# Kernel tuning notes

Measured on AMD Instinct MI355X. Metric: run time of the kernel, lower is better.

The kernel has to match this reference:

```python
import jax, jax.numpy as jnp
import numpy as np
from jax import lax

H = 64  # hidden size


def _lstm_layer(x, w_ih, w_hh, b_ih, b_hh):
    """Single LSTM layer, batch_first x: [B, T, D] -> [B, T, H].
    PyTorch gate order: i, f, g, o."""
    B = x.shape[0]
    # Precompute input projections for all timesteps: [T, B, 4H]
    xg = jnp.einsum('btd,gd->tbg', x, w_ih) + (b_ih + b_hh)

    def step(carry, xg_t):
        h, c = carry
        gates = xg_t + h @ w_hh.T  # [B, 4H]
        i, f, g, o = jnp.split(gates, 4, axis=-1)
        i = jax.nn.sigmoid(i)
        f = jax.nn.sigmoid(f)
        g = jnp.tanh(g)
        o = jax.nn.sigmoid(o)
        c = f * c + i * g
        h = o * jnp.tanh(c)
        return (h, c), h

    h0 = jnp.zeros((B, H), dtype=x.dtype)
    c0 = jnp.zeros((B, H), dtype=x.dtype)
    (_, _), hs = lax.scan(step, (h0, c0), xg)  # hs: [T, B, H]
    return jnp.swapaxes(hs, 0, 1)  # [B, T, H]


def setup_inputs() -> dict:
    key = jax.random.key(0)
    ks = jax.random.split(key, 11)
    s = 1.0 / np.sqrt(H)  # PyTorch LSTM init scale
    x = jax.random.normal(ks[0], (8192, 168, 7), dtype=jnp.float32)
    return {
        'x': x,
        'w_ih0': jax.random.normal(ks[1], (4 * H, 7), jnp.float32) * s,
        'w_hh0': jax.random.normal(ks[2], (4 * H, H), jnp.float32) * s,
        'b_ih0': jax.random.normal(ks[3], (4 * H,), jnp.float32) * s,
        'b_hh0': jax.random.normal(ks[4], (4 * H,), jnp.float32) * s,
        'w_ih1': jax.random.normal(ks[5], (4 * H, H), jnp.float32) * s,
        'w_hh1': jax.random.normal(ks[6], (4 * H, H), jnp.float32) * s,
        'b_ih1': jax.random.normal(ks[7], (4 * H,), jnp.float32) * s,
        'b_hh1': jax.random.normal(ks[8], (4 * H,), jnp.float32) * s,
        'fc_w': jax.random.normal(ks[9], (4, H), jnp.float32) * s,
        'fc_b': jax.random.normal(ks[10], (4,), jnp.float32) * s,
    }


def reference(x, w_ih0, w_hh0, b_ih0, b_hh0, w_ih1, w_hh1, b_ih1, b_hh1, fc_w, fc_b):
    h1 = _lstm_layer(x, w_ih0, w_hh0, b_ih0, b_hh0)   # [B, T, H]
    h2 = _lstm_layer(h1, w_ih1, w_hh1, b_ih1, b_hh1)  # [B, T, H]
    last = h2[:, -1, :]                               # dropout is identity in eval
    return last @ fc_w.T + fc_b                       # [B, 4]
```

## Files before the change

### kernel.cpp

```cpp
#include <hip/hip_runtime.h>

#define TT 168
#define HH 64
#define DD 7
#define NS 16
#define BB 8192
#define CH 8
#define NTH 512

typedef float f32x2 __attribute__((ext_vector_type(2)));
typedef float f32x4 __attribute__((ext_vector_type(4)));
typedef _Float16 f16x8 __attribute__((ext_vector_type(8)));

#define MFMA16F(A, B, C) __builtin_amdgcn_mfma_f32_16x16x32_f16((A), (B), (C), 0, 0, 0)

__device__ __forceinline__ f16x8 pack8(f32x4 a, f32x4 b) {
    f16x8 r;
#pragma unroll
    for (int e = 0; e < 4; ++e) { r[e] = (_Float16)a[e]; r[4 + e] = (_Float16)b[e]; }
    return r;
}

__device__ __forceinline__ f32x2 exp2x2(f32x2 a) {
    return (f32x2){__builtin_amdgcn_exp2f(fminf(a.x, 40.0f)),
                   __builtin_amdgcn_exp2f(fminf(a.y, 40.0f))};
}
__device__ __forceinline__ f32x2 rcpx2(f32x2 a) {
    return (f32x2){__builtin_amdgcn_rcpf(a.x), __builtin_amdgcn_rcpf(a.y)};
}

__device__ __forceinline__ void cell_pair(f32x2 si, f32x2 sf, f32x2 sg, f32x2 so,
                                          f32x2& cs, unsigned& dpk) {
    const f32x2 one = {1.0f, 1.0f};
    const f32x2 ui  = exp2x2(si);
    const f32x2 uf  = exp2x2(sf);
    const f32x2 ug  = exp2x2(sg);
    const f32x2 opf = one + uf;
    const f32x2 pig = (one + ui) * (one + ug);
    const f32x2 R1  = rcpx2(pig * opf);
    const f32x2 fv  = pig * R1;
    const f32x2 igs = (ug * 2.88539008f - (f32x2){2.88539008f, 2.88539008f}) * (opf * R1);
    cs = fv * cs + igs;
    const f32x2 uo = exp2x2(so);
    const f32x2 uc = exp2x2(cs);
    const f32x2 R2 = rcpx2((one + uo) * (one + uc));
    const f32x2 hv = (one - uc) * R2;
    asm("v_cvt_pkrtz_f16_f32 %0, %1, %2" : "=v"(dpk) : "v"(hv.x), "v"(hv.y));
}

__device__ __forceinline__ void cell_update(const f32x4& gi, const f32x4& gf,
                                            const f32x4& gg, const f32x4& go,
                                            f32x4& cs, _Float16* dst) {
    f32x2 csA = {cs[0], cs[1]}, csB = {cs[2], cs[3]};
    unsigned d0, d1;
    cell_pair((f32x2){gi[0], gi[1]}, (f32x2){gf[0], gf[1]},
              (f32x2){gg[0], gg[1]}, (f32x2){go[0], go[1]}, csA, d0);
    cell_pair((f32x2){gi[2], gi[3]}, (f32x2){gf[2], gf[3]},
              (f32x2){gg[2], gg[3]}, (f32x2){go[2], go[3]}, csB, d1);
    cs[0] = csA.x; cs[1] = csA.y; cs[2] = csB.x; cs[3] = csB.y;
    *(uint2*)dst = make_uint2(d0, d1);
}

__global__ __launch_bounds__(NTH, 4)
void weather_lstm_mfma(const float* __restrict__ x,
                       const float* __restrict__ w_ih0, const float* __restrict__ w_hh0,
                       const float* __restrict__ b_ih0, const float* __restrict__ b_hh0,
                       const float* __restrict__ w_ih1, const float* __restrict__ w_hh1,
                       const float* __restrict__ b_ih1, const float* __restrict__ b_hh1,
                       const float* __restrict__ fc_w, const float* __restrict__ fc_b,
                       float* __restrict__ out)
{
    __shared__ f16x8 xs[2][CH][4][NS];
    __shared__ __align__(16) _Float16 h1[2][NS][72];
    __shared__ __align__(16) _Float16 h2[2][NS][72];

    const int tid  = threadIdx.x;
    const int wv   = tid >> 6;
    const int q    = wv & 3;
    const int lane = tid & 63;
    const int col  = lane & 15;
    const int kg   = lane >> 4;
    const int s0   = blockIdx.x * NS;
    const int ub   = 16 * q + 4 * kg;

    for (int i = tid; i < 2 * NS * 72; i += NTH) {
        ((short*)h1)[i] = 0; ((short*)h2)[i] = 0;
    }
    {
        const f16x8 z8i = {0, 0, 0, 0, 0, 0, 0, 0};
        f16x8* xf = &xs[0][0][0][0];
        for (int i = tid; i < 2 * CH * 4 * NS; i += NTH) xf[i] = z8i;
    }
    __syncthreads();
    if (tid < CH * NS) {
        const int tloc = tid >> 4, ss = tid & 15;
        const float* px = x + ((size_t)(s0 + ss) * TT + tloc) * DD;
        f32x4 a, b;
        a[0] = px[0]; a[1] = px[1]; a[2] = px[2]; a[3] = px[3];
        b[0] = px[4]; b[1] = px[5]; b[2] = px[6]; b[3] = 1.0f;
        xs[0][tloc][0][ss] = pack8(a, b);
    }
    __syncthreads();

    const f32x4 zz = {0, 0, 0, 0};

    if (wv < 4) {
        f16x8 W0[4][2], WX[4];
#pragma unroll
        for (int t4 = 0; t4 < 4; ++t4) {
            const float sc = (t4 == 2) ? -2.88539008f : -1.44269504f;
            const int row = 64 * t4 + 16 * q + col;
#pragma unroll
            for (int kf = 0; kf < 2; ++kf) {
                const float* p = w_hh0 + (size_t)row * HH + 32 * kf + 8 * kg;
                W0[t4][kf] = pack8(*(const f32x4*)p * sc, *(const f32x4*)(p + 4) * sc);
            }
            f32x4 a = {0, 0, 0, 0}, b = {0, 0, 0, 0};
            if (kg == 0) {
                const float* p = w_ih0 + (size_t)row * DD;
                a[0] = p[0]; a[1] = p[1]; a[2] = p[2]; a[3] = p[3];
                b[0] = p[4]; b[1] = p[5]; b[2] = p[6];
                b[3] = b_ih0[row] + b_hh0[row];
            }
            WX[t4] = pack8(a * sc, b * sc);
        }
        f32x4 c1 = {0, 0, 0, 0};

        const f16x8* xk = &xs[0][0][kg][col];
        const _Float16* r0a = &h1[0][col][8 * kg];
        const _Float16* r0b = &h1[0][col][32 + 8 * kg];
        const _Float16* r1a = &h1[1][col][8 * kg];
        const _Float16* r1b = &h1[1][col][32 + 8 * kg];
        _Float16* wp0 = &h1[0][col][ub];
        _Float16* wp1 = &h1[1][col][ub];

        auto l0_step = [&](int xofs, const _Float16* ra, const _Float16* rb,
                           _Float16* wr) {
            f32x4 a0, a1, a2, a3;
            const f16x8 ax = xk[xofs];
            a0 = MFMA16F(WX[0], ax, zz);
            a1 = MFMA16F(WX[1], ax, zz);
            a2 = MFMA16F(WX[2], ax, zz);
            a3 = MFMA16F(WX[3], ax, zz);
            f16x8 dh = *(const f16x8*)ra;
            a0 = MFMA16F(W0[0][0], dh, a0);
            a1 = MFMA16F(W0[1][0], dh, a1);
            a2 = MFMA16F(W0[2][0], dh, a2);
            a3 = MFMA16F(W0[3][0], dh, a3);
            dh = *(const f16x8*)rb;
            a0 = MFMA16F(W0[0][1], dh, a0);
            a1 = MFMA16F(W0[1][1], dh, a1);
            a2 = MFMA16F(W0[2][1], dh, a2);
            a3 = MFMA16F(W0[3][1], dh, a3);
            cell_update(a0, a1, a2, a3, c1, wr);
        };
        auto refill = [&](int kref) {
            if (tid < CH * NS) {
                const int tloc = tid >> 4, ss = tid & 15;
                const int tg = kref + CH + tloc;
                const float* px = x + ((size_t)(s0 + ss) * TT + tg) * DD;
                f32x4 a, b;
                a[0] = px[0]; a[1] = px[1]; a[2] = px[2]; a[3] = px[3];
                b[0] = px[4]; b[1] = px[5]; b[2] = px[6]; b[3] = 1.0f;
                const int nb = ((kref >> 3) & 1) ^ 1;
                xs[nb][tloc][0][ss] = pack8(a, b);
            }
        };

        refill(0);
        l0_step(0, r1a, r1b, wp0);
        __syncthreads();
        l0_step(64, r0a, r0b, wp1);
        __syncthreads();

#pragma unroll 1
        for (int j = 1; j < 84; ++j) {
            const int xofs = ((2 * j) & 15) * 64;
            if ((j & 3) == 0 && j < 80) refill(2 * j);
            l0_step(xofs, r1a, r1b, wp0);
            __syncthreads();
            l0_step(xofs + 64, r0a, r0b, wp1);
            __syncthreads();
        }
        __syncthreads();
    } else {
        f16x8 W1[4][4];
        f32x4 bias1[4];
#pragma unroll
        for (int t4 = 0; t4 < 4; ++t4) {
            const float sc = (t4 == 2) ? -2.88539008f : -1.44269504f;
            const int row = 64 * t4 + 16 * q + col;
            const int rr  = 64 * t4 + 16 * q + 4 * kg;
            bias1[t4] = (*(const f32x4*)(b_ih1 + rr) + *(const f32x4*)(b_hh1 + rr)) * sc;
#pragma unroll
            for (int kf = 0; kf < 4; ++kf) {
                const float* base = (kf < 2) ? (w_ih1 + (size_t)row * HH + 32 * kf)
                                             : (w_hh1 + (size_t)row * HH + 32 * (kf - 2));
                const float* p = base + 8 * kg;
                W1[t4][kf] = pack8(*(const f32x4*)p * sc, *(const f32x4*)(p + 4) * sc);
            }
        }
        f32x4 c2 = {0, 0, 0, 0};

        const _Float16* p1a0 = &h1[0][col][8 * kg];
        const _Float16* p1b0 = &h1[0][col][32 + 8 * kg];
        const _Float16* p1a1 = &h1[1][col][8 * kg];
        const _Float16* p1b1 = &h1[1][col][32 + 8 * kg];
        const _Float16* p2a0 = &h2[0][col][8 * kg];
        const _Float16* p2b0 = &h2[0][col][32 + 8 * kg];
        const _Float16* p2a1 = &h2[1][col][8 * kg];
        const _Float16* p2b1 = &h2[1][col][32 + 8 * kg];
        _Float16* q0 = &h2[0][col][ub];
        _Float16* q1 = &h2[1][col][ub];

        auto l1_step = [&](const _Float16* ha, const _Float16* hb,
                           const _Float16* ea, const _Float16* eb, _Float16* wr) {
            f32x4 a0, a1, a2, a3;
            f16x8 dh = *(const f16x8*)ha;
            a0 = MFMA16F(W1[0][0], dh, bias1[0]);
            a1 = MFMA16F(W1[1][0], dh, bias1[1]);
            a2 = MFMA16F(W1[2][0], dh, bias1[2]);
            a3 = MFMA16F(W1[3][0], dh, bias1[3]);
            dh = *(const f16x8*)hb;
            a0 = MFMA16F(W1[0][1], dh, a0);
            a1 = MFMA16F(W1[1][1], dh, a1);
            a2 = MFMA16F(W1[2][1], dh, a2);
            a3 = MFMA16F(W1[3][1], dh, a3);
            dh = *(const f16x8*)ea;
            a0 = MFMA16F(W1[0][2], dh, a0);
            a1 = MFMA16F(W1[1][2], dh, a1);
            a2 = MFMA16F(W1[2][2], dh, a2);
            a3 = MFMA16F(W1[3][2], dh, a3);
            dh = *(const f16x8*)eb;
            a0 = MFMA16F(W1[0][3], dh, a0);
            a1 = MFMA16F(W1[1][3], dh, a1);
            a2 = MFMA16F(W1[2][3], dh, a2);
            a3 = MFMA16F(W1[3][3], dh, a3);
            cell_update(a0, a1, a2, a3, c2, wr);
        };

        __syncthreads();
        l1_step(p1a0, p1b0, p2a1, p2b1, q0);
        __syncthreads();

#pragma unroll 1
        for (int j = 1; j < 84; ++j) {
            l1_step(p1a1, p1b1, p2a0, p2b0, q1);
            __syncthreads();
            l1_step(p1a0, p1b0, p2a1, p2b1, q0);
            __syncthreads();
        }
        l1_step(p1a1, p1b1, p2a0, p2b0, q1);
        __syncthreads();
    }

    if (tid < NS * 4) {
        const int s = tid >> 2, k = tid & 3;
        float a = fc_b[k];
#pragma unroll
        for (int j = 0; j < HH; ++j)
            a = fmaf((float)h2[1][s][j], fc_w[k * HH + j], a);
        out[(size_t)(s0 + s) * 4 + k] = a;
    }
}

extern "C" void kernel_launch(void* const* d_in, const int* in_sizes, int n_in,
                              void* d_out, int out_size, void* d_ws, size_t ws_size,
                              hipStream_t stream) {
    const float* x     = (const float*)d_in[0];
    const float* w_ih0 = (const float*)d_in[1];
    const float* w_hh0 = (const float*)d_in[2];
    const float* b_ih0 = (const float*)d_in[3];
    const float* b_hh0 = (const float*)d_in[4];
    const float* w_ih1 = (const float*)d_in[5];
    const float* w_hh1 = (const float*)d_in[6];
    const float* b_ih1 = (const float*)d_in[7];
    const float* b_hh1 = (const float*)d_in[8];
    const float* fc_w  = (const float*)d_in[9];
    const float* fc_b  = (const float*)d_in[10];
    float* out = (float*)d_out;

    dim3 grid(BB / NS), block(NTH);
    weather_lstm_mfma<<<grid, block, 0, stream>>>(
        x, w_ih0, w_hh0, b_ih0, b_hh0,
        w_ih1, w_hh1, b_ih1, b_hh1, fc_w, fc_b, out);
}
```

Baseline: 225.8 us.

## Split each LSTM layer across eight waves with interleaved gate rows per MFMA

Doubles the block to 1024 threads so each layer uses eight waves instead of four. Each wave now computes eight hidden units per step, with two gates interleaved into each 16-row MFMA tile, so every wave issues half as many MFMAs and one cell_pair per step. The goal is to shorten the serial per-timestep critical path by spreading the recurrence over more waves. The cost is lower occupancy per CU, a barrier across twice as many waves, and narrower 4-byte LDS writes.

```diff
diff --git a/kernel.cpp b/kernel.cpp
--- a/kernel.cpp
+++ b/kernel.cpp
@@ -6,7 +6,7 @@
 #define NS 16
 #define BB 8192
 #define CH 8
-#define NTH 512
+#define NTH 1024
 
 typedef float f32x2 __attribute__((ext_vector_type(2)));
 typedef float f32x4 __attribute__((ext_vector_type(4)));
@@ -48,20 +48,7 @@
     asm("v_cvt_pkrtz_f16_f32 %0, %1, %2" : "=v"(dpk) : "v"(hv.x), "v"(hv.y));
 }
 
-__device__ __forceinline__ void cell_update(const f32x4& gi, const f32x4& gf,
-                                            const f32x4& gg, const f32x4& go,
-                                            f32x4& cs, _Float16* dst) {
-    f32x2 csA = {cs[0], cs[1]}, csB = {cs[2], cs[3]};
-    unsigned d0, d1;
-    cell_pair((f32x2){gi[0], gi[1]}, (f32x2){gf[0], gf[1]},
-              (f32x2){gg[0], gg[1]}, (f32x2){go[0], go[1]}, csA, d0);
-    cell_pair((f32x2){gi[2], gi[3]}, (f32x2){gf[2], gf[3]},
-              (f32x2){gg[2], gg[3]}, (f32x2){go[2], go[3]}, csB, d1);
-    cs[0] = csA.x; cs[1] = csA.y; cs[2] = csB.x; cs[3] = csB.y;
-    *(uint2*)dst = make_uint2(d0, d1);
-}
-
-__global__ __launch_bounds__(NTH, 4)
+__global__ __launch_bounds__(NTH, 8)
 void weather_lstm_mfma(const float* __restrict__ x,
                        const float* __restrict__ w_ih0, const float* __restrict__ w_hh0,
                        const float* __restrict__ b_ih0, const float* __restrict__ b_hh0,
@@ -76,12 +63,12 @@
 
     const int tid  = threadIdx.x;
     const int wv   = tid >> 6;
-    const int q    = wv & 3;
+    const int u    = wv & 7;
     const int lane = tid & 63;
     const int col  = lane & 15;
     const int kg   = lane >> 4;
     const int s0   = blockIdx.x * NS;
-    const int ub   = 16 * q + 4 * kg;
+    const int uw   = 8 * u + 2 * kg;
 
     for (int i = tid; i < 2 * NS * 72; i += NTH) {
         ((short*)h1)[i] = 0; ((short*)h2)[i] = 0;
@@ -104,16 +91,17 @@
 
     const f32x4 zz = {0, 0, 0, 0};
 
-    if (wv < 4) {
-        f16x8 W0[4][2], WX[4];
-#pragma unroll
-        for (int t4 = 0; t4 < 4; ++t4) {
-            const float sc = (t4 == 2) ? -2.88539008f : -1.44269504f;
-            const int row = 64 * t4 + 16 * q + col;
+    if (wv < 8) {
+        f16x8 W0[2][2], WX[2];
+#pragma unroll
+        for (int t = 0; t < 2; ++t) {
+            const int gsel = 2 * t + (col & 1);
+            const float sc = (gsel == 2) ? -2.88539008f : -1.44269504f;
+            const int row = 64 * gsel + 8 * u + (col >> 1);
 #pragma unroll
             for (int kf = 0; kf < 2; ++kf) {
                 const float* p = w_hh0 + (size_t)row * HH + 32 * kf + 8 * kg;
-                W0[t4][kf] = pack8(*(const f32x4*)p * sc, *(const f32x4*)(p + 4) * sc);
+                W0[t][kf] = pack8(*(const f32x4*)p * sc, *(const f32x4*)(p + 4) * sc);
             }
             f32x4 a = {0, 0, 0, 0}, b = {0, 0, 0, 0};
             if (kg == 0) {
@@ -122,37 +110,30 @@
                 b[0] = p[4]; b[1] = p[5]; b[2] = p[6];
                 b[3] = b_ih0[row] + b_hh0[row];
             }
-            WX[t4] = pack8(a * sc, b * sc);
-        }
-        f32x4 c1 = {0, 0, 0, 0};
+            WX[t] = pack8(a * sc, b * sc);
+        }
+        f32x2 cs = {0, 0};
 
         const f16x8* xk = &xs[0][0][kg][col];
-        const _Float16* r0a = &h1[0][col][8 * kg];
-        const _Float16* r0b = &h1[0][col][32 + 8 * kg];
-        const _Float16* r1a = &h1[1][col][8 * kg];
-        const _Float16* r1b = &h1[1][col][32 + 8 * kg];
-        _Float16* wp0 = &h1[0][col][ub];
-        _Float16* wp1 = &h1[1][col][ub];
-
-        auto l0_step = [&](int xofs, const _Float16* ra, const _Float16* rb,
-                           _Float16* wr) {
-            f32x4 a0, a1, a2, a3;
+        const _Float16* r0 = &h1[0][col][8 * kg];
+        const _Float16* r1 = r0 + NS * 72;
+        unsigned* wp0 = (unsigned*)&h1[0][col][uw];
+        unsigned* wp1 = (unsigned*)((_Float16*)wp0 + NS * 72);
+
+        auto l0_step = [&](int xofs, const _Float16* r, unsigned* wr) {
             const f16x8 ax = xk[xofs];
-            a0 = MFMA16F(WX[0], ax, zz);
-            a1 = MFMA16F(WX[1], ax, zz);
-            a2 = MFMA16F(WX[2], ax, zz);
-            a3 = MFMA16F(WX[3], ax, zz);
-            f16x8 dh = *(const f16x8*)ra;
-            a0 = MFMA16F(W0[0][0], dh, a0);
-            a1 = MFMA16F(W0[1][0], dh, a1);
-            a2 = MFMA16F(W0[2][0], dh, a2);
-            a3 = MFMA16F(W0[3][0], dh, a3);
-            dh = *(const f16x8*)rb;
-            a0 = MFMA16F(W0[0][1], dh, a0);
-            a1 = MFMA16F(W0[1][1], dh, a1);
-            a2 = MFMA16F(W0[2][1], dh, a2);
-            a3 = MFMA16F(W0[3][1], dh, a3);
-            cell_update(a0, a1, a2, a3, c1, wr);
+            f32x4 aP = MFMA16F(WX[0], ax, zz);
+            f32x4 aQ = MFMA16F(WX[1], ax, zz);
+            f16x8 dh = *(const f16x8*)r;
+            aP = MFMA16F(W0[0][0], dh, aP);
+            aQ = MFMA16F(W0[1][0], dh, aQ);
+            dh = *(const f16x8*)(r + 32);
+            aP = MFMA16F(W0[0][1], dh, aP);
+            aQ = MFMA16F(W0[1][1], dh, aQ);
+            unsigned dpk;
+            cell_pair((f32x2){aP[0], aP[2]}, (f32x2){aP[1], aP[3]},
+                      (f32x2){aQ[0], aQ[2]}, (f32x2){aQ[1], aQ[3]}, cs, dpk);
+            *wr = dpk;
         };
         auto refill = [&](int kref) {
             if (tid < CH * NS) {
@@ -168,89 +149,84 @@
         };
 
         refill(0);
-        l0_step(0, r1a, r1b, wp0);
-        __syncthreads();
-        l0_step(64, r0a, r0b, wp1);
+        l0_step(0, r1, wp0);
+        __syncthreads();
+        l0_step(64, r0, wp1);
         __syncthreads();
 
 #pragma unroll 1
         for (int j = 1; j < 84; ++j) {
             const int xofs = ((2 * j) & 15) * 64;
             if ((j & 3) == 0 && j < 80) refill(2 * j);
-            l0_step(xofs, r1a, r1b, wp0);
-            __syncthreads();
-            l0_step(xofs + 64, r0a, r0b, wp1);
+            l0_step(xofs, r1, wp0);
+            __syncthreads();
+            l0_step(xofs + 64, r0, wp1);
             __syncthreads();
         }
         __syncthreads();
     } else {
-        f16x8 W1[4][4];
-        f32x4 bias1[4];
-#pragma unroll
-        for (int t4 = 0; t4 < 4; ++t4) {
-            const float sc = (t4 == 2) ? -2.88539008f : -1.44269504f;
-            const int row = 64 * t4 + 16 * q + col;
-            const int rr  = 64 * t4 + 16 * q + 4 * kg;
-            bias1[t4] = (*(const f32x4*)(b_ih1 + rr) + *(const f32x4*)(b_hh1 + rr)) * sc;
+        f16x8 W1[2][4];
+        f32x4 bias1[2];
+#pragma unroll
+        for (int t = 0; t < 2; ++t) {
+            const int gsel = 2 * t + (col & 1);
+            const float sc = (gsel == 2) ? -2.88539008f : -1.44269504f;
+            const int row = 64 * gsel + 8 * u + (col >> 1);
 #pragma unroll
             for (int kf = 0; kf < 4; ++kf) {
                 const float* base = (kf < 2) ? (w_ih1 + (size_t)row * HH + 32 * kf)
                                              : (w_hh1 + (size_t)row * HH + 32 * (kf - 2));
                 const float* p = base + 8 * kg;
-                W1[t4][kf] = pack8(*(const f32x4*)p * sc, *(const f32x4*)(p + 4) * sc);
-            }
-        }
-        f32x4 c2 = {0, 0, 0, 0};
-
-        const _Float16* p1a0 = &h1[0][col][8 * kg];
-        const _Float16* p1b0 = &h1[0][col][32 + 8 * kg];
-        const _Float16* p1a1 = &h1[1][col][8 * kg];
-        const _Float16* p1b1 = &h1[1][col][32 + 8 * kg];
-        const _Float16* p2a0 = &h2[0][col][8 * kg];
-        const _Float16* p2b0 = &h2[0][col][32 + 8 * kg];
-        const _Float16* p2a1 = &h2[1][col][8 * kg];
-        const _Float16* p2b1 = &h2[1][col][32 + 8 * kg];
-        _Float16* q0 = &h2[0][col][ub];
-        _Float16* q1 = &h2[1][col][ub];
-
-        auto l1_step = [&](const _Float16* ha, const _Float16* hb,
-                           const _Float16* ea, const _Float16* eb, _Float16* wr) {
-            f32x4 a0, a1, a2, a3;
-            f16x8 dh = *(const f16x8*)ha;
-            a0 = MFMA16F(W1[0][0], dh, bias1[0]);
-            a1 = MFMA16F(W1[1][0], dh, bias1[1]);
-            a2 = MFMA16F(W1[2][0], dh, bias1[2]);
-            a3 = MFMA16F(W1[3][0], dh, bias1[3]);
-            dh = *(const f16x8*)hb;
-            a0 = MFMA16F(W1[0][1], dh, a0);
-            a1 = MFMA16F(W1[1][1], dh, a1);
-            a2 = MFMA16F(W1[2][1], dh, a2);
-            a3 = MFMA16F(W1[3][1], dh, a3);
-            dh = *(const f16x8*)ea;
-            a0 = MFMA16F(W1[0][2], dh, a0);
-            a1 = MFMA16F(W1[1][2], dh, a1);
-            a2 = MFMA16F(W1[2][2], dh, a2);
-            a3 = MFMA16F(W1[3][2], dh, a3);
-            dh = *(const f16x8*)eb;
-            a0 = MFMA16F(W1[0][3], dh, a0);
-            a1 = MFMA16F(W1[1][3], dh, a1);
-            a2 = MFMA16F(W1[2][3], dh, a2);
-            a3 = MFMA16F(W1[3][3], dh, a3);
-            cell_update(a0, a1, a2, a3, c2, wr);
+                W1[t][kf] = pack8(*(const f32x4*)p * sc, *(const f32x4*)(p + 4) * sc);
+            }
+#pragma unroll
+            for (int e = 0; e < 4; ++e) {
+                const int g2 = 2 * t + (e & 1);
+                const float sce = (g2 == 2) ? -2.88539008f : -1.44269504f;
+                const int br = 64 * g2 + 8 * u + 2 * kg + (e >> 1);
+                bias1[t][e] = (b_ih1[br] + b_hh1[br]) * sce;
+            }
+        }
+        f32x2 cs = {0, 0};
+
+        const _Float16* p10 = &h1[0][col][8 * kg];
+        const _Float16* p11 = p10 + NS * 72;
+        const _Float16* p20 = &h2[0][col][8 * kg];
+        const _Float16* p21 = p20 + NS * 72;
+        unsigned* q0 = (unsigned*)&h2[0][col][uw];
+        unsigned* q1 = (unsigned*)((_Float16*)q0 + NS * 72);
+
+        auto l1_step = [&](const _Float16* h1p, const _Float16* h2p, unsigned* wr) {
+            f16x8 dh = *(const f16x8*)h1p;
+            f32x4 aP = MFMA16F(W1[0][0], dh, bias1[0]);
+            f32x4 aQ = MFMA16F(W1[1][0], dh, bias1[1]);
+            dh = *(const f16x8*)(h1p + 32);
+            aP = MFMA16F(W1[0][1], dh, aP);
+            aQ = MFMA16F(W1[1][1], dh, aQ);
+            dh = *(const f16x8*)h2p;
+            aP = MFMA16F(W1[0][2], dh, aP);
+            aQ = MFMA16F(W1[1][2], dh, aQ);
+            dh = *(const f16x8*)(h2p + 32);
+            aP = MFMA16F(W1[0][3], dh, aP);
+            aQ = MFMA16F(W1[1][3], dh, aQ);
+            unsigned dpk;
+            cell_pair((f32x2){aP[0], aP[2]}, (f32x2){aP[1], aP[3]},
+                      (f32x2){aQ[0], aQ[2]}, (f32x2){aQ[1], aQ[3]}, cs, dpk);
+            *wr = dpk;
         };
 
         __syncthreads();
-        l1_step(p1a0, p1b0, p2a1, p2b1, q0);
+        l1_step(p10, p21, q0);
         __syncthreads();
 
 #pragma unroll 1
         for (int j = 1; j < 84; ++j) {
-            l1_step(p1a1, p1b1, p2a0, p2b0, q1);
-            __syncthreads();
-            l1_step(p1a0, p1b0, p2a1, p2b1, q0);
-            __syncthreads();
-        }
-        l1_step(p1a1, p1b1, p2a0, p2b0, q1);
+            l1_step(p11, p20, q1);
+            __syncthreads();
+            l1_step(p10, p21, q0);
+            __syncthreads();
+        }
+        l1_step(p11, p20, q1);
         __syncthreads();
     }
 
```

Result: no change. 227.1 us (+0.6%).
